# Kernel tuning notes

Hardware: AMD Instinct MI355X
Metric: run time of the kernel (lower is better)

Reference implementation:

```python
import jax, jax.numpy as jnp
import numpy as np

TEMPERATURE = 1.0        # sample_codebook_temperature
COMMITMENT_COST = 1.0

B, T, D, K = 8, 4096, 64, 1024


def setup_inputs() -> dict:
    key = jax.random.key(0)
    k1, k2 = jax.random.split(key)
    x = jax.random.normal(k1, (B, T, D), dtype=jnp.float32)
    embeddings = jax.random.normal(k2, (D, K), dtype=jnp.float32)  # (embedding_dim, codebook_size)
    return {"x": x, "embeddings": embeddings}


def gumbel_softmax(logits, temperature):
    # logits: [N, K]
    K_ = logits.shape[1]
    indices = jnp.argmax(logits, axis=1)
    enc = jax.nn.one_hot(indices, K_, dtype=logits.dtype)
    pi0 = jax.nn.softmax(logits, axis=-1)
    pi1 = (enc + jax.nn.softmax(logits / temperature, axis=-1)) / 2
    pi1 = jax.nn.softmax(jax.lax.stop_gradient(jnp.log(pi1) - logits), axis=1)
    pi2 = 2 * pi1 - 0.5 * pi0
    encodings = pi2 - jax.lax.stop_gradient(pi2) + enc  # straight-through encodings
    return indices, encodings


def reference(x, embeddings):
    D_, K_ = embeddings.shape
    flat = x.reshape(-1, D_)                              # [N, D]
    # squared euclidean distances via matmul (cdist trick)
    sim = flat @ embeddings                               # [N, K]
    dist = (jnp.sum(flat ** 2, axis=1, keepdims=True)
            - 2.0 * sim
            + jnp.sum(embeddings ** 2, axis=0, keepdims=True))
    indices, encodings = gumbel_softmax(-dist, TEMPERATURE)
    indices = indices.reshape(x.shape[:-1])               # [B, T]
    quantized = embeddings.T[indices]                     # gather: [B, T, D]
    e_latent_loss = jnp.mean(jnp.square(jax.lax.stop_gradient(quantized) - x))
    loss = e_latent_loss * COMMITMENT_COST
    # straight-through estimator (training-mode output; same values as eval)
    quantized = x + jax.lax.stop_gradient(quantized - x)
    return quantized, encodings, indices, loss
```

## Files before the change

kernel.cpp:

```cpp
#include <hip/hip_runtime.h>
#include <hip/hip_bf16.h>


#define NROWS 32768
#define DDIM  64
#define KCB   1024
#define MARGIN 0.02f

typedef float    f32x4 __attribute__((ext_vector_type(4)));
typedef _Float16 f16x8 __attribute__((ext_vector_type(8)));

#define WS_ET    0
#define WS_H     65536
#define WS_PART  66560
#define WS_EHI   67584
#define WS_ELO   100352

__global__ __launch_bounds__(64) void kA_prep(const float* __restrict__ E,
                                              float* __restrict__ Et,
                                              float* __restrict__ h,
                                              _Float16* __restrict__ Ehi,
                                              _Float16* __restrict__ Elo) {
  int k = blockIdx.x * 64 + threadIdx.x;
  float col[DDIM];
  float sum = 0.f;
#pragma unroll
  for (int d = 0; d < DDIM; ++d) {
    float v = E[d * KCB + k];
    col[d] = v;
    sum = fmaf(v, v, sum);
  }
  float4* dst = (float4*)(Et + (size_t)k * DDIM);
#pragma unroll
  for (int i = 0; i < 16; ++i)
    dst[i] = make_float4(col[4*i], col[4*i+1], col[4*i+2], col[4*i+3]);
  h[k] = 0.5f * sum;

#pragma unroll
  for (int w = 0; w < 2; ++w) {
    f16x8 hi8[4], lo8[4];
#pragma unroll
    for (int p = 0; p < 32; ++p) {
      int dl = w * 32 + 4 * (p >> 3) + (p & 3) + 16 * ((p >> 2) & 1);
      float v = col[dl];
      _Float16 hi = (_Float16)v;
      hi8[p >> 3][p & 7] = hi;
      lo8[p >> 3][p & 7] = (_Float16)(v - (float)hi);
    }
#pragma unroll
    for (int q = 0; q < 4; ++q) {
      *(f16x8*)(Ehi + (size_t)k * DDIM + w * 32 + q * 8) = hi8[q];
      *(f16x8*)(Elo + (size_t)k * DDIM + w * 32 + q * 8) = lo8[q];
    }
  }
}

__global__ __launch_bounds__(128, 2) void kB_main(const float* __restrict__ x,
                                                  const _Float16* __restrict__ Ehi,
                                                  const _Float16* __restrict__ Elo,
                                                  const float* __restrict__ Et,
                                                  const float* __restrict__ h,
                                                  float* __restrict__ partial,
                                                  float* __restrict__ out_q,
                                                  float* __restrict__ out_enc,
                                                  float* __restrict__ out_ind) {
  __shared__ float mb1[2][32], mb2[2][32];
  __shared__ int   mi1[2][32];
  __shared__ int   sidx[32];
  __shared__ int   flags[32];
  __shared__ int   nflag;
  __shared__ float rb[2];
  __shared__ int   ri[2];
  __shared__ float red[2];

  int tid  = threadIdx.x;
  int ws   = tid >> 6;
  int lane = tid & 63;
  int g = lane >> 4, c = lane & 15;
  int r0 = blockIdx.x * 32;

  if (tid == 0) nflag = 0;

  f16x8 Ahi[2][2], Alo[2][2];
#pragma unroll
  for (int r = 0; r < 2; ++r) {
    const float* xb = x + (size_t)(r0 + r * 16 + c) * DDIM;
#pragma unroll
    for (int w = 0; w < 2; ++w) {
      f32x4 xa = *(const f32x4*)(xb + w * 32 + 4 * g);
      f32x4 xc = *(const f32x4*)(xb + w * 32 + 16 + 4 * g);
#pragma unroll
      for (int e = 0; e < 4; ++e) {
        _Float16 hi = (_Float16)xa[e];
        Ahi[r][w][e] = hi;
        Alo[r][w][e] = (_Float16)(xa[e] - (float)hi);
      }
#pragma unroll
      for (int e = 0; e < 4; ++e) {
        _Float16 hi = (_Float16)xc[e];
        Ahi[r][w][4 + e] = hi;
        Alo[r][w][4 + e] = (_Float16)(xc[e] - (float)hi);
      }
    }
  }

  float b1[2][4], b2[2][4];
  int   i1[2][4];
#pragma unroll
  for (int r = 0; r < 2; ++r)
#pragma unroll
    for (int q = 0; q < 4; ++q) { b1[r][q] = -3.0e38f; b2[r][q] = -3.0e38f; i1[r][q] = 0; }

  const _Float16* peh = Ehi + (size_t)(ws * 512 + c) * DDIM + g * 8;
  const _Float16* pel = Elo + (size_t)(ws * 512 + c) * DDIM + g * 8;

  f16x8 bh0n = *(const f16x8*)(peh);
  f16x8 bl0n = *(const f16x8*)(pel);
  f16x8 bh1n = *(const f16x8*)(peh + 32);
  f16x8 bl1n = *(const f16x8*)(pel + 32);
  float hn = h[ws * 512 + c];

  for (int ch = 0; ch < 32; ++ch) {
    f16x8 bh0 = bh0n, bl0 = bl0n, bh1 = bh1n, bl1 = bl1n;
    float hc = hn;
    if (ch < 31) {
      size_t off = (size_t)(ch + 1) * 16 * DDIM;
      bh0n = *(const f16x8*)(peh + off);
      bl0n = *(const f16x8*)(pel + off);
      bh1n = *(const f16x8*)(peh + off + 32);
      bl1n = *(const f16x8*)(pel + off + 32);
      hn = h[ws * 512 + (ch + 1) * 16 + c];
    }
    int code = ws * 512 + ch * 16 + c;
#pragma unroll
    for (int r = 0; r < 2; ++r) {
      f32x4 a = { -hc, -hc, -hc, -hc };
      a = __builtin_amdgcn_mfma_f32_16x16x32_f16(Alo[r][0], bh0, a, 0, 0, 0);
      a = __builtin_amdgcn_mfma_f32_16x16x32_f16(Ahi[r][0], bl0, a, 0, 0, 0);
      a = __builtin_amdgcn_mfma_f32_16x16x32_f16(Ahi[r][0], bh0, a, 0, 0, 0);
      a = __builtin_amdgcn_mfma_f32_16x16x32_f16(Alo[r][1], bh1, a, 0, 0, 0);
      a = __builtin_amdgcn_mfma_f32_16x16x32_f16(Ahi[r][1], bl1, a, 0, 0, 0);
      a = __builtin_amdgcn_mfma_f32_16x16x32_f16(Ahi[r][1], bh1, a, 0, 0, 0);
#pragma unroll
      for (int q = 0; q < 4; ++q) {
        float s = a[q];
        bool gt = s > b1[r][q];
        b2[r][q] = gt ? b1[r][q] : fmaxf(b2[r][q], s);
        i1[r][q] = gt ? code : i1[r][q];
        b1[r][q] = gt ? s : b1[r][q];
      }
    }
  }

#pragma unroll
  for (int step = 1; step <= 8; step <<= 1) {
#pragma unroll
    for (int r = 0; r < 2; ++r)
#pragma unroll
      for (int q = 0; q < 4; ++q) {
        float ob1 = __shfl_xor(b1[r][q], step);
        int   oi1 = __shfl_xor(i1[r][q], step);
        float ob2 = __shfl_xor(b2[r][q], step);
        bool win = (ob1 > b1[r][q]) || (ob1 == b1[r][q] && oi1 < i1[r][q]);
        float loser = win ? b1[r][q] : ob1;
        b1[r][q] = win ? ob1 : b1[r][q];
        i1[r][q] = win ? oi1 : i1[r][q];
        b2[r][q] = fmaxf(fmaxf(b2[r][q], ob2), loser);
      }
  }
  if (c == 0) {
#pragma unroll
    for (int r = 0; r < 2; ++r)
#pragma unroll
      for (int q = 0; q < 4; ++q) {
        int row = r * 16 + 4 * g + q;
        mb1[ws][row] = b1[r][q];
        mi1[ws][row] = i1[r][q];
        mb2[ws][row] = b2[r][q];
      }
  }
  __syncthreads();

  if (tid < 32) {
    float a1 = mb1[0][tid], a2 = mb1[1][tid];
    int   j1 = mi1[0][tid], j2 = mi1[1][tid];
    bool w1 = (a2 > a1) || (a2 == a1 && j2 < j1);
    float bb1 = w1 ? a2 : a1;
    int   ii1 = w1 ? j2 : j1;
    float bb2 = fmaxf(fmaxf(mb2[0][tid], mb2[1][tid]), w1 ? a1 : a2);
    sidx[tid] = ii1;
    if (bb1 - bb2 <= MARGIN) { int p = atomicAdd(&nflag, 1); flags[p] = tid; }
  }
  __syncthreads();

  int nf = nflag;
  for (int fi = 0; fi < nf; ++fi) {
    int row = flags[fi];
    int n = r0 + row;
    const f32x4* xr = (const f32x4*)(x + (size_t)n * DDIM);
    f32x4 xv[16];
#pragma unroll
    for (int d = 0; d < 16; ++d) xv[d] = xr[d];
    float best = -3.0e38f; int bi = 0;
#pragma unroll 1
    for (int j = 0; j < 8; ++j) {
      int code = j * 128 + tid;
      const f32x4* er = (const f32x4*)(Et + (size_t)code * DDIM);
      float acc = -h[code];
#pragma unroll
      for (int d = 0; d < 16; ++d) {
        f32x4 e4 = er[d], x4 = xv[d];
        acc = fmaf(x4[0], e4[0], acc); acc = fmaf(x4[1], e4[1], acc);
        acc = fmaf(x4[2], e4[2], acc); acc = fmaf(x4[3], e4[3], acc);
      }
      if (acc > best || (acc == best && code < bi)) { best = acc; bi = code; }
    }
#pragma unroll
    for (int step = 1; step <= 32; step <<= 1) {
      float ob = __shfl_xor(best, step);
      int   oi = __shfl_xor(bi, step);
      if (ob > best || (ob == best && oi < bi)) { best = ob; bi = oi; }
    }
    if (lane == 0) { rb[ws] = best; ri[ws] = bi; }
    __syncthreads();
    if (tid == 0) {
      bool w1 = (rb[1] > rb[0]) || (rb[1] == rb[0] && ri[1] < ri[0]);
      sidx[row] = w1 ? ri[1] : ri[0];
    }
    __syncthreads();
  }

  if (tid < 32) out_ind[r0 + tid] = (float)sidx[tid];

  float lsum = 0.f;
#pragma unroll
  for (int i = 0; i < 4; ++i) {
    int f = tid + i * 128;
    int row = f >> 4, cc = f & 15;
    int n = r0 + row;
    int bi = sidx[row];
    f32x4 q4 = *(const f32x4*)(Et + (size_t)bi * DDIM + cc * 4);
    f32x4 x4 = *(const f32x4*)(x + (size_t)n * DDIM + cc * 4);
    float d0 = q4[0] - x4[0], d1 = q4[1] - x4[1], d2 = q4[2] - x4[2], d3 = q4[3] - x4[3];
    lsum = fmaf(d0, d0, lsum); lsum = fmaf(d1, d1, lsum);
    lsum = fmaf(d2, d2, lsum); lsum = fmaf(d3, d3, lsum);
    __builtin_nontemporal_store(q4, (f32x4*)(out_q + (size_t)n * DDIM + cc * 4));
  }

#pragma unroll 1
  for (int rr = 0; rr < 32; ++rr) {
    int bk = sidx[rr];
    float* rowp = out_enc + (size_t)(r0 + rr) * KCB;
#pragma unroll
    for (int i = 0; i < 2; ++i) {
      int slot = tid + i * 128;
      f32x4 v = (f32x4)(0.f);
      if ((bk >> 2) == slot) v[bk & 3] = 1.0f;
      __builtin_nontemporal_store(v, (f32x4*)(rowp + slot * 4));
    }
  }

#pragma unroll
  for (int off = 32; off > 0; off >>= 1) lsum += __shfl_down(lsum, off);
  if (lane == 0) red[ws] = lsum;
  __syncthreads();
  if (tid == 0) partial[blockIdx.x] = red[0] + red[1];
}

__global__ void k5_loss(const float* __restrict__ partial, float* __restrict__ out_loss) {
  int t = threadIdx.x;
  float s = 0.f;
#pragma unroll
  for (int i = 0; i < 4; ++i) s += partial[t + i * 256];
#pragma unroll
  for (int off = 32; off > 0; off >>= 1) s += __shfl_down(s, off);
  __shared__ float red[4];
  int lane = t & 63, w = t >> 6;
  if (lane == 0) red[w] = s;
  __syncthreads();
  if (t == 0) out_loss[0] = (red[0] + red[1] + red[2] + red[3]) * (1.0f / 2097152.0f);
}

extern "C" void kernel_launch(void* const* d_in, const int* in_sizes, int n_in,
                              void* d_out, int out_size, void* d_ws, size_t ws_size,
                              hipStream_t stream) {
  const float* x = (const float*)d_in[0];
  const float* E = (const float*)d_in[1];

  float* ws   = (float*)d_ws;
  float* Et   = ws + WS_ET;
  float* h    = ws + WS_H;
  float* part = ws + WS_PART;
  _Float16* Ehi = (_Float16*)(ws + WS_EHI);
  _Float16* Elo = (_Float16*)(ws + WS_ELO);

  float* out      = (float*)d_out;
  float* out_q    = out;
  float* out_enc  = out + 2097152;
  float* out_ind  = out + 35651584;
  float* out_loss = out + 35684352;

  kA_prep<<<16, 64, 0, stream>>>(E, Et, h, Ehi, Elo);
  kB_main<<<1024, 128, 0, stream>>>(x, Ehi, Elo, Et, h, part, out_q, out_enc, out_ind);
  k5_loss<<<1, 256, 0, stream>>>(part, out_loss);
}
```

Baseline: 220.3 us.

## Split work into 16-row blocks with four waves each covering a codebook quarter

The main kernel now handles 16 rows per block with 256 threads. Each of the four waves scans a quarter of the codebook instead of half, and the grid doubles to 2048 blocks. The register prefetch of the next codebook chunk is removed, the loop is no longer unrolled, and launch bounds ask for higher occupancy, so latency is hidden by more waves instead of software pipelining. The trade-off is that each block re-reads the full codebook for only 16 rows, which doubles codebook traffic per row, and the cross-wave merge adds more reduction steps. The workspace offsets and the loss reduction are adjusted for the larger partial buffer.

```diff
diff --git a/kernel.cpp b/kernel.cpp
--- a/kernel.cpp
+++ b/kernel.cpp
@@ -13,8 +13,8 @@
 #define WS_ET    0
 #define WS_H     65536
 #define WS_PART  66560
-#define WS_EHI   67584
-#define WS_ELO   100352
+#define WS_EHI   68608
+#define WS_ELO   101376
 
 __global__ __launch_bounds__(64) void kA_prep(const float* __restrict__ E,
                                               float* __restrict__ Et,
@@ -55,7 +55,7 @@
   }
 }
 
-__global__ __launch_bounds__(128, 2) void kB_main(const float* __restrict__ x,
+__global__ __launch_bounds__(256, 8) void kB_main(const float* __restrict__ x,
                                                   const _Float16* __restrict__ Ehi,
                                                   const _Float16* __restrict__ Elo,
                                                   const float* __restrict__ Et,
@@ -64,27 +64,26 @@
                                                   float* __restrict__ out_q,
                                                   float* __restrict__ out_enc,
                                                   float* __restrict__ out_ind) {
-  __shared__ float mb1[2][32], mb2[2][32];
-  __shared__ int   mi1[2][32];
-  __shared__ int   sidx[32];
-  __shared__ int   flags[32];
+  __shared__ float mb1[4][16], mb2[4][16];
+  __shared__ int   mi1[4][16];
+  __shared__ int   sidx[16];
+  __shared__ int   flags[16];
   __shared__ int   nflag;
-  __shared__ float rb[2];
-  __shared__ int   ri[2];
-  __shared__ float red[2];
+  __shared__ float rbw[4];
+  __shared__ int   riw[4];
+  __shared__ float red[4];
 
   int tid  = threadIdx.x;
-  int ws   = tid >> 6;
+  int wq   = tid >> 6;
   int lane = tid & 63;
   int g = lane >> 4, c = lane & 15;
-  int r0 = blockIdx.x * 32;
+  int r0 = blockIdx.x * 16;
 
   if (tid == 0) nflag = 0;
 
-  f16x8 Ahi[2][2], Alo[2][2];
-#pragma unroll
-  for (int r = 0; r < 2; ++r) {
-    const float* xb = x + (size_t)(r0 + r * 16 + c) * DDIM;
+  f16x8 Ahi[2], Alo[2];
+  {
+    const float* xb = x + (size_t)(r0 + c) * DDIM;
 #pragma unroll
     for (int w = 0; w < 2; ++w) {
       f32x4 xa = *(const f32x4*)(xb + w * 32 + 4 * g);
@@ -92,124 +91,109 @@
 #pragma unroll
       for (int e = 0; e < 4; ++e) {
         _Float16 hi = (_Float16)xa[e];
-        Ahi[r][w][e] = hi;
-        Alo[r][w][e] = (_Float16)(xa[e] - (float)hi);
+        Ahi[w][e] = hi;
+        Alo[w][e] = (_Float16)(xa[e] - (float)hi);
       }
 #pragma unroll
       for (int e = 0; e < 4; ++e) {
         _Float16 hi = (_Float16)xc[e];
-        Ahi[r][w][4 + e] = hi;
-        Alo[r][w][4 + e] = (_Float16)(xc[e] - (float)hi);
-      }
-    }
-  }
-
-  float b1[2][4], b2[2][4];
-  int   i1[2][4];
-#pragma unroll
-  for (int r = 0; r < 2; ++r)
-#pragma unroll
-    for (int q = 0; q < 4; ++q) { b1[r][q] = -3.0e38f; b2[r][q] = -3.0e38f; i1[r][q] = 0; }
-
-  const _Float16* peh = Ehi + (size_t)(ws * 512 + c) * DDIM + g * 8;
-  const _Float16* pel = Elo + (size_t)(ws * 512 + c) * DDIM + g * 8;
-
-  f16x8 bh0n = *(const f16x8*)(peh);
-  f16x8 bl0n = *(const f16x8*)(pel);
-  f16x8 bh1n = *(const f16x8*)(peh + 32);
-  f16x8 bl1n = *(const f16x8*)(pel + 32);
-  float hn = h[ws * 512 + c];
-
-  for (int ch = 0; ch < 32; ++ch) {
-    f16x8 bh0 = bh0n, bl0 = bl0n, bh1 = bh1n, bl1 = bl1n;
-    float hc = hn;
-    if (ch < 31) {
-      size_t off = (size_t)(ch + 1) * 16 * DDIM;
-      bh0n = *(const f16x8*)(peh + off);
-      bl0n = *(const f16x8*)(pel + off);
-      bh1n = *(const f16x8*)(peh + off + 32);
-      bl1n = *(const f16x8*)(pel + off + 32);
-      hn = h[ws * 512 + (ch + 1) * 16 + c];
-    }
-    int code = ws * 512 + ch * 16 + c;
-#pragma unroll
-    for (int r = 0; r < 2; ++r) {
-      f32x4 a = { -hc, -hc, -hc, -hc };
-      a = __builtin_amdgcn_mfma_f32_16x16x32_f16(Alo[r][0], bh0, a, 0, 0, 0);
-      a = __builtin_amdgcn_mfma_f32_16x16x32_f16(Ahi[r][0], bl0, a, 0, 0, 0);
-      a = __builtin_amdgcn_mfma_f32_16x16x32_f16(Ahi[r][0], bh0, a, 0, 0, 0);
-      a = __builtin_amdgcn_mfma_f32_16x16x32_f16(Alo[r][1], bh1, a, 0, 0, 0);
-      a = __builtin_amdgcn_mfma_f32_16x16x32_f16(Ahi[r][1], bl1, a, 0, 0, 0);
-      a = __builtin_amdgcn_mfma_f32_16x16x32_f16(Ahi[r][1], bh1, a, 0, 0, 0);
-#pragma unroll
-      for (int q = 0; q < 4; ++q) {
-        float s = a[q];
-        bool gt = s > b1[r][q];
-        b2[r][q] = gt ? b1[r][q] : fmaxf(b2[r][q], s);
-        i1[r][q] = gt ? code : i1[r][q];
-        b1[r][q] = gt ? s : b1[r][q];
-      }
+        Ahi[w][4 + e] = hi;
+        Alo[w][4 + e] = (_Float16)(xc[e] - (float)hi);
+      }
+    }
+  }
+
+  float b1[4], b2[4];
+  int   i1[4];
+#pragma unroll
+  for (int q = 0; q < 4; ++q) { b1[q] = -3.0e38f; b2[q] = -3.0e38f; i1[q] = 0; }
+
+  const _Float16* peh = Ehi + (size_t)(wq * 256 + c) * DDIM + g * 8;
+  const _Float16* pel = Elo + (size_t)(wq * 256 + c) * DDIM + g * 8;
+
+#pragma unroll 1
+  for (int ch = 0; ch < 16; ++ch) {
+    size_t off = (size_t)ch * 16 * DDIM;
+    f16x8 bh0 = *(const f16x8*)(peh + off);
+    f16x8 bl0 = *(const f16x8*)(pel + off);
+    f16x8 bh1 = *(const f16x8*)(peh + off + 32);
+    f16x8 bl1 = *(const f16x8*)(pel + off + 32);
+    float hc = h[wq * 256 + ch * 16 + c];
+    int code = wq * 256 + ch * 16 + c;
+    f32x4 a = { -hc, -hc, -hc, -hc };
+    a = __builtin_amdgcn_mfma_f32_16x16x32_f16(Alo[0], bh0, a, 0, 0, 0);
+    a = __builtin_amdgcn_mfma_f32_16x16x32_f16(Ahi[0], bl0, a, 0, 0, 0);
+    a = __builtin_amdgcn_mfma_f32_16x16x32_f16(Ahi[0], bh0, a, 0, 0, 0);
+    a = __builtin_amdgcn_mfma_f32_16x16x32_f16(Alo[1], bh1, a, 0, 0, 0);
+    a = __builtin_amdgcn_mfma_f32_16x16x32_f16(Ahi[1], bl1, a, 0, 0, 0);
+    a = __builtin_amdgcn_mfma_f32_16x16x32_f16(Ahi[1], bh1, a, 0, 0, 0);
+#pragma unroll
+    for (int q = 0; q < 4; ++q) {
+      float s = a[q];
+      bool gt = s > b1[q];
+      b2[q] = gt ? b1[q] : fmaxf(b2[q], s);
+      i1[q] = gt ? code : i1[q];
+      b1[q] = gt ? s : b1[q];
     }
   }
 
 #pragma unroll
   for (int step = 1; step <= 8; step <<= 1) {
 #pragma unroll
-    for (int r = 0; r < 2; ++r)
-#pragma unroll
-      for (int q = 0; q < 4; ++q) {
-        float ob1 = __shfl_xor(b1[r][q], step);
-        int   oi1 = __shfl_xor(i1[r][q], step);
-        float ob2 = __shfl_xor(b2[r][q], step);
-        bool win = (ob1 > b1[r][q]) || (ob1 == b1[r][q] && oi1 < i1[r][q]);
-        float loser = win ? b1[r][q] : ob1;
-        b1[r][q] = win ? ob1 : b1[r][q];
-        i1[r][q] = win ? oi1 : i1[r][q];
-        b2[r][q] = fmaxf(fmaxf(b2[r][q], ob2), loser);
-      }
+    for (int q = 0; q < 4; ++q) {
+      float ob1 = __shfl_xor(b1[q], step);
+      int   oi1 = __shfl_xor(i1[q], step);
+      float ob2 = __shfl_xor(b2[q], step);
+      bool win = (ob1 > b1[q]) || (ob1 == b1[q] && oi1 < i1[q]);
+      float loser = win ? b1[q] : ob1;
+      b1[q] = win ? ob1 : b1[q];
+      i1[q] = win ? oi1 : i1[q];
+      b2[q] = fmaxf(fmaxf(b2[q], ob2), loser);
+    }
   }
   if (c == 0) {
 #pragma unroll
-    for (int r = 0; r < 2; ++r)
-#pragma unroll
-      for (int q = 0; q < 4; ++q) {
-        int row = r * 16 + 4 * g + q;
-        mb1[ws][row] = b1[r][q];
-        mi1[ws][row] = i1[r][q];
-        mb2[ws][row] = b2[r][q];
-      }
-  }
-  __syncthreads();
-
-  if (tid < 32) {
-    float a1 = mb1[0][tid], a2 = mb1[1][tid];
-    int   j1 = mi1[0][tid], j2 = mi1[1][tid];
-    bool w1 = (a2 > a1) || (a2 == a1 && j2 < j1);
-    float bb1 = w1 ? a2 : a1;
-    int   ii1 = w1 ? j2 : j1;
-    float bb2 = fmaxf(fmaxf(mb2[0][tid], mb2[1][tid]), w1 ? a1 : a2);
+    for (int q = 0; q < 4; ++q) {
+      int row = 4 * g + q;
+      mb1[wq][row] = b1[q];
+      mi1[wq][row] = i1[q];
+      mb2[wq][row] = b2[q];
+    }
+  }
+  __syncthreads();
+
+  if (tid < 16) {
+    float bb1 = mb1[0][tid], bb2 = mb2[0][tid];
+    int   ii1 = mi1[0][tid];
+#pragma unroll
+    for (int qd = 1; qd < 4; ++qd) {
+      float a1 = mb1[qd][tid];
+      int   j1 = mi1[qd][tid];
+      bool w1 = (a1 > bb1) || (a1 == bb1 && j1 < ii1);
+      bb2 = fmaxf(fmaxf(bb2, mb2[qd][tid]), w1 ? bb1 : a1);
+      bb1 = w1 ? a1 : bb1;
+      ii1 = w1 ? j1 : ii1;
+    }
     sidx[tid] = ii1;
     if (bb1 - bb2 <= MARGIN) { int p = atomicAdd(&nflag, 1); flags[p] = tid; }
   }
   __syncthreads();
 
   int nf = nflag;
+#pragma unroll 1
   for (int fi = 0; fi < nf; ++fi) {
     int row = flags[fi];
     int n = r0 + row;
-    const f32x4* xr = (const f32x4*)(x + (size_t)n * DDIM);
-    f32x4 xv[16];
-#pragma unroll
-    for (int d = 0; d < 16; ++d) xv[d] = xr[d];
     float best = -3.0e38f; int bi = 0;
 #pragma unroll 1
-    for (int j = 0; j < 8; ++j) {
-      int code = j * 128 + tid;
+    for (int j = 0; j < 4; ++j) {
+      int code = j * 256 + tid;
       const f32x4* er = (const f32x4*)(Et + (size_t)code * DDIM);
+      const f32x4* xr = (const f32x4*)(x + (size_t)n * DDIM);
       float acc = -h[code];
 #pragma unroll
       for (int d = 0; d < 16; ++d) {
-        f32x4 e4 = er[d], x4 = xv[d];
+        f32x4 e4 = er[d], x4 = xr[d];
         acc = fmaf(x4[0], e4[0], acc); acc = fmaf(x4[1], e4[1], acc);
         acc = fmaf(x4[2], e4[2], acc); acc = fmaf(x4[3], e4[3], acc);
       }
@@ -221,57 +205,56 @@
       int   oi = __shfl_xor(bi, step);
       if (ob > best || (ob == best && oi < bi)) { best = ob; bi = oi; }
     }
-    if (lane == 0) { rb[ws] = best; ri[ws] = bi; }
+    if (lane == 0) { rbw[wq] = best; riw[wq] = bi; }
     __syncthreads();
     if (tid == 0) {
-      bool w1 = (rb[1] > rb[0]) || (rb[1] == rb[0] && ri[1] < ri[0]);
-      sidx[row] = w1 ? ri[1] : ri[0];
+      float bb = rbw[0]; int ii = riw[0];
+#pragma unroll
+      for (int qd = 1; qd < 4; ++qd) {
+        bool w1 = (rbw[qd] > bb) || (rbw[qd] == bb && riw[qd] < ii);
+        bb = w1 ? rbw[qd] : bb;
+        ii = w1 ? riw[qd] : ii;
+      }
+      sidx[row] = ii;
     }
     __syncthreads();
   }
 
-  if (tid < 32) out_ind[r0 + tid] = (float)sidx[tid];
-
-  float lsum = 0.f;
-#pragma unroll
-  for (int i = 0; i < 4; ++i) {
-    int f = tid + i * 128;
-    int row = f >> 4, cc = f & 15;
+  if (tid < 16) out_ind[r0 + tid] = (float)sidx[tid];
+
+  float lsum;
+  {
+    int row = tid >> 4, cc = tid & 15;
     int n = r0 + row;
     int bi = sidx[row];
     f32x4 q4 = *(const f32x4*)(Et + (size_t)bi * DDIM + cc * 4);
     f32x4 x4 = *(const f32x4*)(x + (size_t)n * DDIM + cc * 4);
     float d0 = q4[0] - x4[0], d1 = q4[1] - x4[1], d2 = q4[2] - x4[2], d3 = q4[3] - x4[3];
-    lsum = fmaf(d0, d0, lsum); lsum = fmaf(d1, d1, lsum);
-    lsum = fmaf(d2, d2, lsum); lsum = fmaf(d3, d3, lsum);
+    lsum = d0 * d0;
+    lsum = fmaf(d1, d1, lsum); lsum = fmaf(d2, d2, lsum); lsum = fmaf(d3, d3, lsum);
     __builtin_nontemporal_store(q4, (f32x4*)(out_q + (size_t)n * DDIM + cc * 4));
   }
 
 #pragma unroll 1
-  for (int rr = 0; rr < 32; ++rr) {
+  for (int rr = 0; rr < 16; ++rr) {
     int bk = sidx[rr];
-    float* rowp = out_enc + (size_t)(r0 + rr) * KCB;
-#pragma unroll
-    for (int i = 0; i < 2; ++i) {
-      int slot = tid + i * 128;
-      f32x4 v = (f32x4)(0.f);
-      if ((bk >> 2) == slot) v[bk & 3] = 1.0f;
-      __builtin_nontemporal_store(v, (f32x4*)(rowp + slot * 4));
-    }
+    f32x4 v = (f32x4)(0.f);
+    if ((bk >> 2) == tid) v[bk & 3] = 1.0f;
+    __builtin_nontemporal_store(v, (f32x4*)(out_enc + (size_t)(r0 + rr) * KCB + tid * 4));
   }
 
 #pragma unroll
   for (int off = 32; off > 0; off >>= 1) lsum += __shfl_down(lsum, off);
-  if (lane == 0) red[ws] = lsum;
-  __syncthreads();
-  if (tid == 0) partial[blockIdx.x] = red[0] + red[1];
+  if (lane == 0) red[wq] = lsum;
+  __syncthreads();
+  if (tid == 0) partial[blockIdx.x] = red[0] + red[1] + red[2] + red[3];
 }
 
 __global__ void k5_loss(const float* __restrict__ partial, float* __restrict__ out_loss) {
   int t = threadIdx.x;
   float s = 0.f;
 #pragma unroll
-  for (int i = 0; i < 4; ++i) s += partial[t + i * 256];
+  for (int i = 0; i < 8; ++i) s += partial[t + i * 256];
 #pragma unroll
   for (int off = 32; off > 0; off >>= 1) s += __shfl_down(s, off);
   __shared__ float red[4];
@@ -301,6 +284,6 @@
   float* out_loss = out + 35684352;
 
   kA_prep<<<16, 64, 0, stream>>>(E, Et, h, Ehi, Elo);
-  kB_main<<<1024, 128, 0, stream>>>(x, Ehi, Elo, Et, h, part, out_q, out_enc, out_ind);
+  kB_main<<<2048, 256, 0, stream>>>(x, Ehi, Elo, Et, h, part, out_q, out_enc, out_ind);
   k5_loss<<<1, 256, 0, stream>>>(part, out_loss);
 }
```

After: 240.3 us. 9.1% more time.
